# Kernel tuning notes

Measured on AMD Instinct MI355X. Metric: run time of the kernel, lower is better.

The kernel has to match this reference:

```python
import jax, jax.numpy as jnp
import numpy as np

N_PATCHES = 32
PATCH = 128
EPS = 1e-12


def _sample_and_gather(attention, WSI):
    B, Ha, Wa = attention.shape
    _, C, H, W = WSI.shape
    # --- categorical sampling WITHOUT replacement via Gumbel top-k ---
    flat = attention.reshape(B, Ha * Wa)
    probs = flat / jnp.sum(flat, axis=-1, keepdims=True)  # use_logits=False: map is already positive weights
    logp = jnp.log(probs + EPS)
    u = jax.random.uniform(jax.random.key(42), logp.shape, dtype=logp.dtype)
    gumbel = -jnp.log(-jnp.log(u + EPS) + EPS)
    _, idx = jax.lax.top_k(jax.lax.stop_gradient(logp) + gumbel, N_PATCHES)  # [B, N]
    sampled_attention = jnp.take_along_axis(probs, idx, axis=-1)  # [B, N], differentiable w.r.t. attention
    # --- map attention-grid indices to high-res top-left corners ---
    rows, cols = idx // Wa, idx % Wa
    sh, sw = H // Ha, W // Wa  # low->high scale (receptive_field=0)
    y0 = jnp.clip(rows * sh + (sh - PATCH) // 2, 0, H - PATCH)
    x0 = jnp.clip(cols * sw + (sw - PATCH) // 2, 0, W - PATCH)
    # --- gather fixed-size crops: vmap over patches, then over batch ---
    def crop(img, y, x):  # img: [C, H, W]
        return jax.lax.dynamic_slice(img, (0, y, x), (C, PATCH, PATCH))
    patches = jax.vmap(lambda img, ys, xs: jax.vmap(lambda y, x: crop(img, y, x))(ys, xs))(WSI, y0, x0)
    return patches, sampled_attention  # [B, N, C, PATCH, PATCH], [B, N]


def setup_inputs() -> dict:
    key = jax.random.key(0)
    k1, k2, k3, k4 = jax.random.split(key, 4)
    B = 4
    x_low = jax.random.normal(k1, (B, 3, 512, 512), jnp.float32)
    x_high = jax.random.normal(k2, (B, 3, 2048, 2048), jnp.float32)
    WSI = jax.random.normal(k3, (B, 3, 2048, 2048), jnp.float32)
    attention = jax.random.uniform(k4, (B, 64, 64), jnp.float32)
    return {"x_low": x_low, "x_high": x_high, "attention": attention, "WSI": WSI}


def reference(x_low, x_high, attention, WSI):
    # x_low / x_high only define the low->high mapping; the crop source is WSI,
    # matching the original forward which delegates to WSI_sampling(samples, WSI, attention).
    patches, sampled_attention = _sample_and_gather(attention, WSI)
    return patches, sampled_attention
```

## Files before the change

### kernel.cpp

```cpp
#include <hip/hip_runtime.h>
#include <stdint.h>
#include <math.h>


namespace {
constexpr int B      = 4;
constexpr int NP     = 32;
constexpr int PATCH_ = 128;
constexpr int GRID   = 4096;
constexpr int HW     = 2048;
constexpr int NT     = 1024;
constexpr int BPB    = 64;
constexpr int NBLK   = B * BPB;
constexpr int NW     = NT / 64;
constexpr int QP     = GRID / NT;
constexpr int NBIN   = 8192;
constexpr int NCB    = 128;
constexpr int MAXC   = 512;
constexpr int GITER  = 6;
constexpr float EPSF = 1e-12f;

typedef float f32x4 __attribute__((ext_vector_type(4)));

__device__ inline uint32_t rotl32(uint32_t x, uint32_t r){ return (x<<r)|(x>>(32u-r)); }

__device__ inline void threefry2x32_k042(uint32_t x0, uint32_t x1,
                                         uint32_t& o0, uint32_t& o1){
  const uint32_t k0 = 0u, k1 = 42u;
  const uint32_t k2 = k0 ^ k1 ^ 0x1BD11BDAu;
  x0 += k0; x1 += k1;
#define RND(r) { x0 += x1; x1 = rotl32(x1,(r)); x1 ^= x0; }
#define G_A RND(13) RND(15) RND(26) RND(6)
#define G_B RND(17) RND(29) RND(16) RND(24)
  G_A x0 += k1; x1 += k2 + 1u;
  G_B x0 += k2; x1 += k0 + 2u;
  G_A x0 += k0; x1 += k1 + 3u;
  G_B x0 += k1; x1 += k2 + 4u;
  G_A x0 += k2; x1 += k0 + 5u;
#undef G_A
#undef G_B
#undef RND
  o0 = x0; o1 = x1;
}

__device__ inline uint32_t mono_f32(float v){
  const uint32_t bits = __float_as_uint(v);
  return (bits & 0x80000000u) ? ~bits : (bits | 0x80000000u);
}

__device__ inline float u01(uint32_t bits){
  return __uint_as_float((bits >> 9) | 0x3F800000u) - 1.0f;
}

__global__ __launch_bounds__(NT) void fused_sample_gather(
    const float* __restrict__ att, const float* __restrict__ wsi,
    float* __restrict__ out_attn, f32x4* __restrict__ out4){
  const int tid  = threadIdx.x;
  const int wv   = tid >> 6;
  const int lane = tid & 63;
  const int b    = blockIdx.x >> 6;
  const int g    = blockIdx.x & 63;
  __shared__ uint32_t hist[NBIN];
  __shared__ uint32_t coarse[NCB];
  __shared__ float redv[NW];
  __shared__ float ssum;
  __shared__ int   scnt;
  __shared__ int   stcut;
  __shared__ unsigned short candj[MAXC];
  __shared__ unsigned long long dkey[MAXC];
  __shared__ float dprob[MAXC];
  __shared__ int2  gtab[NP];

  const float* a = att + b * GRID;

  const float4 va = reinterpret_cast<const float4*>(a)[tid];
  float areg[QP] = {va.x, va.y, va.z, va.w};

  #pragma unroll
  for (int i = 0; i < NBIN / NT; ++i) hist[i * NT + tid] = 0u;
  if (tid == 0) scnt = 0;

  float local = areg[0] + areg[1] + areg[2] + areg[3];
  #pragma unroll
  for (int d = 1; d < 64; d <<= 1) local += __shfl_xor(local, d, 64);
  if (lane == 0) redv[wv] = local;
  __syncthreads();
  if (tid == 0){
    float s = 0.f;
    #pragma unroll
    for (int w = 0; w < NW; ++w) s += redv[w];
    ssum = s;
  }
  __syncthreads();
  const float sum = ssum;

  uint32_t kreg[QP];
  #pragma unroll
  for (int q = 0; q < QP; ++q){
    const int e = b * GRID + (tid << 2) + q;
    uint32_t o0, o1;
    threefry2x32_k042(0u, (uint32_t)e, o0, o1);
    const float u = u01(o0 ^ o1);
    const float gum = -__logf(-__logf(u + EPSF) + EPSF);
    const float s   = __logf(areg[q] / sum + EPSF) + gum;
    kreg[q] = mono_f32(s);
    atomicAdd(&hist[kreg[q] >> 19], 1u);
  }
  __syncthreads();

  if (tid < NCB){
    uint32_t s = 0;
    #pragma unroll
    for (int i = 0; i < 64; ++i) s += hist[tid * 64 + i];
    coarse[tid] = s;
  }
  __syncthreads();

  if (wv == 0){
    uint32_t vlo = coarse[lane], vhi = coarse[lane + 64];
    #pragma unroll
    for (int d = 1; d < 64; d <<= 1){
      uint32_t t = __shfl_down(vhi, d, 64); if (lane + d < 64) vhi += t;
      t = __shfl_down(vlo, d, 64);          if (lane + d < 64) vlo += t;
    }
    const uint32_t Thi = __shfl(vhi, 0, 64);
    const uint32_t Slo = vlo + Thi;
    const unsigned long long mhi = __ballot(vhi >= (uint32_t)NP);
    const unsigned long long mlo = __ballot(Slo >= (uint32_t)NP);
    const int cstar = mhi ? (64 + (63 - __clzll(mhi))) : (63 - __clzll(mlo));
    const int cn = cstar + 1;
    const uint32_t t1 = __shfl(vhi, (cn - 64) & 63, 64);
    const uint32_t t2 = __shfl(Slo, cn & 63, 64);
    const uint32_t A  = (cn >= 128) ? 0u : ((cn >= 64) ? t1 : t2);
    uint32_t f = hist[cstar * 64 + lane];
    #pragma unroll
    for (int d = 1; d < 64; d <<= 1){
      uint32_t t = __shfl_down(f, d, 64); if (lane + d < 64) f += t;
    }
    const unsigned long long mf = __ballot(A + f >= (uint32_t)NP);
    const int lstar = 63 - __clzll(mf);
    if (lane == 0) stcut = cstar * 64 + lstar - 2;
  }
  __syncthreads();
  const int tcut = stcut;

  #pragma unroll
  for (int q = 0; q < QP; ++q){
    if ((int)(kreg[q] >> 19) >= tcut){
      const int p = atomicAdd(&scnt, 1);
      if (p < MAXC) candj[p] = (unsigned short)((tid << 2) + q);
    }
  }
  __syncthreads();
  const int M = scnt < MAXC ? scnt : MAXC;

  if (tid < M){
    const int j = candj[tid];
    const int e = b * GRID + j;
    uint32_t o0, o1;
    threefry2x32_k042(0u, (uint32_t)e, o0, o1);
    const float u = u01(o0 ^ o1);
    const float gum  = -logf(-logf(u + EPSF) + EPSF);
    const float prob = a[j] / sum;
    const float se   = logf(prob + EPSF) + gum;
    dkey[tid]  = ((unsigned long long)mono_f32(se) << 32)
               | (uint32_t)(GRID - 1 - j);
    dprob[tid] = prob;
  }
  __syncthreads();

  if (tid < M){
    const unsigned long long mk = dkey[tid];
    int rank = 0;
    #pragma unroll 4
    for (int c = 0; c < M; ++c) rank += (dkey[c] > mk) ? 1 : 0;
    if (rank < NP){
      const int j   = GRID - 1 - (int)(uint32_t)(mk & 0xFFFFFFFFull);
      const int row = j >> 6, col = j & 63;
      int y0 = row * 32 - 48; y0 = y0 < 0 ? 0 : (y0 > 1920 ? 1920 : y0);
      int x0 = col * 32 - 48; x0 = x0 < 0 ? 0 : (x0 > 1920 ? 1920 : x0);
      gtab[rank] = make_int2(y0, x0);
      if (g == 0) out_attn[b * NP + rank] = dprob[tid];
    }
  }
  __syncthreads();

  int t = g * NT + tid;
  #pragma unroll
  for (int it = 0; it < GITER; ++it, t += BPB * NT){
    const int l4   = t & 31;
    const int rowb = t >> 5;
    const int r    = rowb & 127;
    const int tmp  = rowb >> 7;
    const int c    = tmp % 3;
    const int n    = tmp / 3;
    const int2 yx  = gtab[n];
    const size_t off = ((size_t)((b * 3 + c) * HW + yx.x + r)) * HW + (size_t)yx.y;
    const f32x4 v = *reinterpret_cast<const f32x4*>(wsi + off + (size_t)l4 * 4);
    __builtin_nontemporal_store(v, out4 + ((size_t)b * 12288 + rowb) * 32 + l4);
  }
}
}

extern "C" void kernel_launch(void* const* d_in, const int* in_sizes, int n_in,
                              void* d_out, int out_size, void* d_ws, size_t ws_size,
                              hipStream_t stream) {
  const float* att = (const float*)d_in[2];
  const float* wsi = (const float*)d_in[3];
  float* out       = (float*)d_out;
  float* out_attn  = out + (size_t)B * NP * 3 * PATCH_ * PATCH_;

  fused_sample_gather<<<NBLK, NT, 0, stream>>>(att, wsi, out_attn, (f32x4*)out);
}
```

Baseline: 19.66 us.

## Pad histogram to avoid bank conflicts and fold candidate scoring into selection

New measurement: 20.58 us. +4.7%, slower.

```diff
diff --git a/kernel.cpp b/kernel.cpp
--- a/kernel.cpp
+++ b/kernel.cpp
@@ -14,7 +14,8 @@
 constexpr int NBLK   = B * BPB;
 constexpr int NW     = NT / 64;
 constexpr int QP     = GRID / NT;
-constexpr int NBIN   = 8192;
+constexpr int FSTR   = 129;
+constexpr int HWORDS = 64 * FSTR;
 constexpr int NCB    = 128;
 constexpr int MAXC   = 512;
 constexpr int GITER  = 6;
@@ -48,6 +49,8 @@
   return (bits & 0x80000000u) ? ~bits : (bits | 0x80000000u);
 }
 
+__device__ inline int haddr(int f){ return (f & 63) * FSTR + (f >> 6); }
+
 __device__ inline float u01(uint32_t bits){
   return __uint_as_float((bits >> 9) | 0x3F800000u) - 1.0f;
 }
@@ -60,13 +63,11 @@
   const int lane = tid & 63;
   const int b    = blockIdx.x >> 6;
   const int g    = blockIdx.x & 63;
-  __shared__ uint32_t hist[NBIN];
+  __shared__ uint32_t hist[HWORDS];
   __shared__ uint32_t coarse[NCB];
   __shared__ float redv[NW];
-  __shared__ float ssum;
   __shared__ int   scnt;
   __shared__ int   stcut;
-  __shared__ unsigned short candj[MAXC];
   __shared__ unsigned long long dkey[MAXC];
   __shared__ float dprob[MAXC];
   __shared__ int2  gtab[NP];
@@ -76,8 +77,7 @@
   const float4 va = reinterpret_cast<const float4*>(a)[tid];
   float areg[QP] = {va.x, va.y, va.z, va.w};
 
-  #pragma unroll
-  for (int i = 0; i < NBIN / NT; ++i) hist[i * NT + tid] = 0u;
+  for (int i = tid; i < HWORDS; i += NT) hist[i] = 0u;
   if (tid == 0) scnt = 0;
 
   float local = areg[0] + areg[1] + areg[2] + areg[3];
@@ -85,14 +85,9 @@
   for (int d = 1; d < 64; d <<= 1) local += __shfl_xor(local, d, 64);
   if (lane == 0) redv[wv] = local;
   __syncthreads();
-  if (tid == 0){
-    float s = 0.f;
-    #pragma unroll
-    for (int w = 0; w < NW; ++w) s += redv[w];
-    ssum = s;
-  }
-  __syncthreads();
-  const float sum = ssum;
+  float sum = 0.f;
+  #pragma unroll
+  for (int w = 0; w < NW; ++w) sum += redv[w];
 
   uint32_t kreg[QP];
   #pragma unroll
@@ -104,14 +99,14 @@
     const float gum = -__logf(-__logf(u + EPSF) + EPSF);
     const float s   = __logf(areg[q] / sum + EPSF) + gum;
     kreg[q] = mono_f32(s);
-    atomicAdd(&hist[kreg[q] >> 19], 1u);
+    atomicAdd(&hist[haddr((int)(kreg[q] >> 19))], 1u);
   }
   __syncthreads();
 
   if (tid < NCB){
     uint32_t s = 0;
     #pragma unroll
-    for (int i = 0; i < 64; ++i) s += hist[tid * 64 + i];
+    for (int i = 0; i < 64; ++i) s += hist[i * FSTR + tid];
     coarse[tid] = s;
   }
   __syncthreads();
@@ -132,7 +127,7 @@
     const uint32_t t1 = __shfl(vhi, (cn - 64) & 63, 64);
     const uint32_t t2 = __shfl(Slo, cn & 63, 64);
     const uint32_t A  = (cn >= 128) ? 0u : ((cn >= 64) ? t1 : t2);
-    uint32_t f = hist[cstar * 64 + lane];
+    uint32_t f = hist[lane * FSTR + cstar];
     #pragma unroll
     for (int d = 1; d < 64; d <<= 1){
       uint32_t t = __shfl_down(f, d, 64); if (lane + d < 64) f += t;
@@ -148,26 +143,22 @@
   for (int q = 0; q < QP; ++q){
     if ((int)(kreg[q] >> 19) >= tcut){
       const int p = atomicAdd(&scnt, 1);
-      if (p < MAXC) candj[p] = (unsigned short)((tid << 2) + q);
+      if (p < MAXC){
+        const int j = (tid << 2) + q;
+        uint32_t o0, o1;
+        threefry2x32_k042(0u, (uint32_t)(b * GRID + j), o0, o1);
+        const float u = u01(o0 ^ o1);
+        const float gum  = -logf(-logf(u + EPSF) + EPSF);
+        const float prob = areg[q] / sum;
+        const float se   = logf(prob + EPSF) + gum;
+        dkey[p]  = ((unsigned long long)mono_f32(se) << 32)
+                 | (uint32_t)(GRID - 1 - j);
+        dprob[p] = prob;
+      }
     }
   }
   __syncthreads();
   const int M = scnt < MAXC ? scnt : MAXC;
-
-  if (tid < M){
-    const int j = candj[tid];
-    const int e = b * GRID + j;
-    uint32_t o0, o1;
-    threefry2x32_k042(0u, (uint32_t)e, o0, o1);
-    const float u = u01(o0 ^ o1);
-    const float gum  = -logf(-logf(u + EPSF) + EPSF);
-    const float prob = a[j] / sum;
-    const float se   = logf(prob + EPSF) + gum;
-    dkey[tid]  = ((unsigned long long)mono_f32(se) << 32)
-               | (uint32_t)(GRID - 1 - j);
-    dprob[tid] = prob;
-  }
-  __syncthreads();
 
   if (tid < M){
     const unsigned long long mk = dkey[tid];
```
